# Kernel optimization log

Measured on AMD Instinct MI355X. Metric: run time of the kernel, lower is better.

## Reference

```python
import jax, jax.numpy as jnp
import numpy as np

VAR0, VAR1 = 0.1, 0.2
CONF_THR = 0.02
NMS_THR = 0.4
PRE_K = 5000
POST_K = 750
N = 85680


def setup_inputs() -> dict:
    key = jax.random.key(0)
    k0, k1, k2, k3 = jax.random.split(key, 4)
    return {
        "loc": jax.random.normal(k0, (N, 4), jnp.float32),
        "conf": jax.random.uniform(k1, (N, 2), jnp.float32),
        "landmarks": jax.random.normal(k2, (N, 10), jnp.float32),
        "priors": jax.random.uniform(k3, (N, 4), jnp.float32),
        "img_w": 1920,
        "img_h": 1088,
    }


def _decode_boxes(loc, priors):
    # center-size decode -> xyxy
    cxy = priors[:, :2] + loc[:, :2] * VAR0 * priors[:, 2:]
    wh = priors[:, 2:] * jnp.exp(loc[:, 2:] * VAR1)
    return jnp.concatenate([cxy - wh * 0.5, cxy + wh * 0.5], axis=-1)


def _decode_landmarks(lmk, priors):
    pts = lmk.reshape(-1, 5, 2)                       # [N,5,2]
    out = priors[:, None, :2] + pts * VAR0 * priors[:, None, 2:]
    return out.reshape(-1, 10)


def _pairwise_iou(boxes):
    # boxes: [K,4] xyxy
    area = (boxes[:, 2] - boxes[:, 0]) * (boxes[:, 3] - boxes[:, 1])
    lt = jnp.maximum(boxes[:, None, :2], boxes[None, :, :2])  # [K,K,2]
    rb = jnp.minimum(boxes[:, None, 2:], boxes[None, :, 2:])
    wh = jnp.clip(rb - lt, 0.0)
    inter = wh[..., 0] * wh[..., 1]
    union = area[:, None] + area[None, :] - inter
    return inter / jnp.maximum(union, 1e-12)


def _greedy_nms(boxes, valid, thr):
    # boxes already sorted by descending score; valid marks real candidates.
    K = boxes.shape[0]
    iou = _pairwise_iou(boxes)                         # [K,K]
    idx = jnp.arange(K)

    def body(i, keep):
        suppress = keep[i] & (iou[i] > thr) & (idx > i)
        return keep & ~suppress

    return jax.lax.fori_loop(0, K, body, valid)


def reference(loc, conf, landmarks, priors, img_w, img_h):
    w = jnp.float32(img_w)
    h = jnp.float32(img_h)
    bbox_scale = jnp.array([w, h, w, h], jnp.float32)
    lmk_scale = jnp.tile(jnp.array([w, h], jnp.float32), 5)

    boxes = _decode_boxes(loc, priors) * bbox_scale          # [N,4]
    lmk = _decode_landmarks(landmarks, priors) * lmk_scale   # [N,10]
    scores = conf[:, 1]                                      # [N]

    # confidence filter fused into top-k via -inf masking (static shapes)
    masked = jnp.where(scores > CONF_THR, scores, -jnp.inf)
    top_scores, order = jax.lax.top_k(masked, PRE_K)         # [PRE_K]
    boxes_k = boxes[order]
    lmk_k = lmk[order]
    valid_k = top_scores > CONF_THR

    keep = _greedy_nms(boxes_k, valid_k, NMS_THR)            # [PRE_K] bool

    # compact kept rows (already score-sorted) into fixed [POST_K,15]
    rank = jnp.cumsum(keep) - 1
    rows = jnp.concatenate([boxes_k, top_scores[:, None], lmk_k], axis=1)
    dest = jnp.where(keep & (rank < POST_K), rank, POST_K)   # OOB -> dropped
    out = jnp.zeros((POST_K, 15), jnp.float32).at[dest].set(rows, mode="drop")
    return out
```

## Files before the change

### kernel.cpp

```cpp
#include <hip/hip_runtime.h>
#include <hip/hip_bf16.h>
#include <math.h>

#define N_IN 85680
#define PRE_K 5000
#define POST_K 750
#define NW 79
#define NPAD 5056
#define HSIZE 8192
#define CAND_MAX 8192
#define CONF_THR 0.02f
#define NMS_THR 0.4f
#define BITS_THR 0x3CA3D70Bu
#define NGRP 20

typedef unsigned int u32;
typedef unsigned long long u64;

__device__ __forceinline__ int cbase(int k) { return k * (5088 - 32 * k); }

__device__ __forceinline__ float opaquef(float x) { asm volatile("" : "+v"(x)); return x; }

__device__ __forceinline__ u32 bucket_of(u32 bits) {
    u32 b = (bits - BITS_THR) >> 13;
    return b >= HSIZE ? (HSIZE - 1) : b;
}

__global__ __launch_bounds__(256) void hist_kernel(const float2* __restrict__ conf2,
                                                   u32* __restrict__ hist) {
    __shared__ u32 h[HSIZE];
    for (int b = threadIdx.x; b < HSIZE; b += 256) h[b] = 0u;
    __syncthreads();
    int i = blockIdx.x * 256 + threadIdx.x;
    if (i < N_IN) {
        float s = conf2[i].y;
        if (s > CONF_THR) atomicAdd(&h[bucket_of(__float_as_uint(s))], 1u);
    }
    __syncthreads();
    for (int b = threadIdx.x; b < HSIZE; b += 256) {
        u32 v = h[b];
        if (v) atomicAdd(&hist[b], v);
    }
}

__global__ __launch_bounds__(1024) void scan_kernel(const u32* __restrict__ hist,
                                                    u32* __restrict__ bsel,
                                                    u32* __restrict__ bstart) {
    __shared__ u32 tot[1024];
    int c = threadIdx.x;
    u32 lh[8];
    u32 t = 0;
#pragma unroll
    for (int k = 0; k < 8; ++k) { lh[k] = hist[c * 8 + k]; t += lh[k]; }
    tot[c] = t;
    __syncthreads();
    for (int d = 1; d < 1024; d <<= 1) {
        u32 v = tot[c] + ((c + d < 1024) ? tot[c + d] : 0u);
        __syncthreads();
        tot[c] = v;
        __syncthreads();
    }
    u32 above = (c + 1 < 1024) ? tot[c + 1] : 0u;
    u32 s = above;
    for (int k = 7; k >= 0; --k) { bstart[c * 8 + k] = s; s += lh[k]; }
    if (above < PRE_K && above + t >= PRE_K) {
        u32 cum = above;
        for (int k = 7; k >= 0; --k) {
            cum += lh[k];
            if (cum >= PRE_K) { bsel[0] = (u32)(c * 8 + k); break; }
        }
    }
    if (c == 0 && tot[0] < PRE_K) bsel[0] = 0u;
}

__global__ __launch_bounds__(256) void compact_kernel(const float2* __restrict__ conf2,
                                                      const u32* __restrict__ bsel,
                                                      const u32* __restrict__ bstart,
                                                      u32* __restrict__ bfill,
                                                      u64* __restrict__ cand) {
    int i = blockIdx.x * 256 + threadIdx.x;
    if (i >= N_IN) return;
    float sc = conf2[i].y;
    if (!(sc > CONF_THR)) return;
    u32 bits = __float_as_uint(sc);
    u32 b = bucket_of(bits);
    if (b < bsel[0]) return;
    u32 pos = bstart[b] + atomicAdd(&bfill[b], 1u);
    if (pos < CAND_MAX) cand[pos] = ((u64)bits << 32) | (u64)(u32)(~(u32)i);
}

__global__ __launch_bounds__(256) void rankdec_kernel(const u64* __restrict__ cand,
                                                      const u32* __restrict__ bstart,
                                                      const u32* __restrict__ bfill,
                                                      const u32* __restrict__ bsel,
                                                      const float4* __restrict__ loc4,
                                                      const float4* __restrict__ pri4,
                                                      const float* __restrict__ lmk,
                                                      const int* __restrict__ imw,
                                                      const int* __restrict__ imh,
                                                      float4* __restrict__ rows4,
                                                      float4* __restrict__ boxes,
                                                      u64* __restrict__ validm) {
    u32 bs = bsel[0];
    u32 total = bstart[bs] + bfill[bs];
    if (total > CAND_MAX) total = CAND_MAX;
    float W = (float)(*imw), H = (float)(*imh);
    for (u32 s = blockIdx.x * blockDim.x + threadIdx.x; s < total;
         s += gridDim.x * blockDim.x) {
        u64 key = cand[s];
        u32 b = bucket_of((u32)(key >> 32));
        u32 st = bstart[b];
        u32 en = st + bfill[b];
        if (en > CAND_MAX) en = CAND_MAX;
        u32 r = st;
        for (u32 j = st; j < en; ++j) r += (cand[j] > key) ? 1u : 0u;
        if (r >= PRE_K) continue;
        u32 i = ~(u32)key;
        float score = __uint_as_float((u32)(key >> 32));
        float4 L = loc4[i];
        float4 P = pri4[i];
        float cx = P.x + opaquef((L.x * 0.1f) * P.z);
        float cy = P.y + opaquef((L.y * 0.1f) * P.w);
        float bw = P.z * (float)exp((double)(L.z * 0.2f));
        float bh = P.w * (float)exp((double)(L.w * 0.2f));
        float hw = opaquef(bw * 0.5f), hh = opaquef(bh * 0.5f);
        float x0 = (cx - hw) * W, y0 = (cy - hh) * H;
        float x1 = (cx + hw) * W, y1 = (cy + hh) * H;
        boxes[r] = make_float4(x0, y0, x1, y1);
        float lm[10];
#pragma unroll
        for (int p = 0; p < 5; ++p) {
            float2 q = ((const float2*)lmk)[(size_t)i * 5 + p];
            lm[2 * p]     = (P.x + opaquef((q.x * 0.1f) * P.z)) * W;
            lm[2 * p + 1] = (P.y + opaquef((q.y * 0.1f) * P.w)) * H;
        }
        float4* row = rows4 + (size_t)r * 4;
        row[0] = make_float4(x0, y0, x1, y1);
        row[1] = make_float4(score, lm[0], lm[1], lm[2]);
        row[2] = make_float4(lm[3], lm[4], lm[5], lm[6]);
        row[3] = make_float4(lm[7], lm[8], lm[9], 0.f);
        atomicOr(&validm[r >> 6], 1ull << (r & 63));
    }
}

__global__ __launch_bounds__(64) void mask_kernel(const float4* __restrict__ boxes,
                                                  u64* __restrict__ cmask) {
    int rem = blockIdx.x, rc = 0;
    while (rem >= rc + 1) { rem -= rc + 1; ++rc; }
    int cc = rem;
    __shared__ float4 cb[64];
    int t = threadIdx.x;
    cb[t] = boxes[cc * 64 + t];
    int i = rc * 64 + t;
    float4 bi = boxes[i];
    __syncthreads();
    float areai = (bi.z - bi.x) * (bi.w - bi.y);
    u64 word = 0ull;
#pragma unroll 4
    for (int k = 0; k < 64; ++k) {
        float4 bj = cb[k];
        float areaj = (bj.z - bj.x) * (bj.w - bj.y);
        float ltx = fmaxf(bi.x, bj.x), lty = fmaxf(bi.y, bj.y);
        float rbx = fminf(bi.z, bj.z), rby = fminf(bi.w, bj.w);
        float wx = fmaxf(rbx - ltx, 0.f), wy = fmaxf(rby - lty, 0.f);
        float inter = opaquef(wx * wy);
        float uni = fmaxf(areai + areaj - inter, 1e-12f);
        float iou = inter / uni;
        if (iou > NMS_THR) word |= (1ull << k);
    }
    if (i < PRE_K) cmask[(size_t)(cbase(cc) + (i - 64 * cc))] = word;
}

#define FC(k, q) cmask[(size_t)(cbase(k) + (q) - 64 * (k))]

#define WAITG(need)                                                                   \
    for (;;) {                                                                        \
        u32 d_ = __hip_atomic_load(&doneCnt, __ATOMIC_RELAXED,                        \
                                   __HIP_MEMORY_SCOPE_WORKGROUP);                     \
        if (d_ > (u32)NGRP) { dead = true; break; }                                   \
        if (d_ >= (u32)(need)) break;                                                 \
    }                                                                                 \
    asm volatile("" ::: "memory");

__device__ __forceinline__ u64 nms_solve(u64 valw, u64 sup, u64 dlow) {
    u64 keep = valw & ~__ballot(sup != 0ull);
    for (;;) {
        u64 conm = __ballot((dlow & keep) != 0ull);
        u64 cm = conm & keep;
        if (cm == 0ull) break;
        u64 U = keep & ~conm;
        u64 rem = __ballot((dlow & U) != 0ull) & keep;
        keep &= ~rem;
    }
    return keep;
}

__global__ __launch_bounds__(512) void reduce_scatter_kernel(const u64* __restrict__ cmask,
                                                             const u64* __restrict__ validm,
                                                             const float* __restrict__ rows,
                                                             float* __restrict__ out) {
    int tid = threadIdx.x;
    int g = tid >> 6, lane = tid & 63;
    __shared__ u64 keepAll[96];
    __shared__ u32 totG[32];
    __shared__ u32 doneCnt;
    __shared__ u32 wpref[96];
    for (int k = tid; k < 96; k += 512) keepAll[k] = 0ull;
    if (tid == 0) doneCnt = 0u;
    __syncthreads();
    u64 lmask = (1ull << lane) - 1ull;

    for (int s = 0; s < 3; ++s) {
        int G = s * 8 + g;
        if (G >= NGRP) break;
        int w0 = 4 * G;
        int nwg = NW - w0; if (nwg > 4) nwg = 4;
        int q0 = 64 * w0 + lane;
        int q1 = q0 + 64;
        int q2 = q0 + 128;
        int q3 = (nwg > 3) ? (q0 + 192) : q0;
        u64 t00 = FC(w0, q0);
        u64 t10 = (nwg > 1) ? FC(w0, q1) : 0ull;
        u64 t11 = (nwg > 1) ? FC(w0 + 1, q1) : 0ull;
        u64 t20 = (nwg > 2) ? FC(w0, q2) : 0ull;
        u64 t21 = (nwg > 2) ? FC(w0 + 1, q2) : 0ull;
        u64 t22 = (nwg > 2) ? FC(w0 + 2, q2) : 0ull;
        u64 t30 = (nwg > 3) ? FC(w0, q3) : 0ull;
        u64 t31 = (nwg > 3) ? FC(w0 + 1, q3) : 0ull;
        u64 t32 = (nwg > 3) ? FC(w0 + 2, q3) : 0ull;
        u64 t33 = (nwg > 3) ? FC(w0 + 3, q3) : 0ull;
        u64 v0 = validm[w0];
        u64 v1 = (nwg > 1) ? validm[w0 + 1] : 0ull;
        u64 v2 = (nwg > 2) ? validm[w0 + 2] : 0ull;
        u64 v3 = (nwg > 3) ? validm[w0 + 3] : 0ull;
        u64 sup0 = 0, sup1 = 0, sup2 = 0, sup3 = 0;
        bool dead = false;

        int d0 = 0;
        u64 c00=0,c01=0,c02=0,c03=0,c10=0,c11=0,c12=0,c13=0;
        if (w0 > 0) {
            c00 = FC(0, q0); c01 = FC(0, q1); c02 = FC(0, q2); c03 = FC(0, q3);
            c10 = FC(1, q0); c11 = FC(1, q1); c12 = FC(1, q2); c13 = FC(1, q3);
        }
        asm volatile("" ::: "memory");
        while (d0 < w0) {
            int d1 = d0 + 2;
            u64 n00=0,n01=0,n02=0,n03=0,n10=0,n11=0,n12=0,n13=0;
            if (d1 < w0) {
                n00 = FC(d1, q0);     n01 = FC(d1, q1);     n02 = FC(d1, q2);     n03 = FC(d1, q3);
                n10 = FC(d1 + 1, q0); n11 = FC(d1 + 1, q1); n12 = FC(d1 + 1, q2); n13 = FC(d1 + 1, q3);
            }
            asm volatile("" ::: "memory");
            WAITG(((d0 + 1) >> 2) + 1)
            if (dead) break;
            u64 ka = keepAll[d0], kb = keepAll[d0 + 1];
            sup0 |= (ka & c00) | (kb & c10);
            sup1 |= (ka & c01) | (kb & c11);
            sup2 |= (ka & c02) | (kb & c12);
            sup3 |= (ka & c03) | (kb & c13);
            c00=n00;c01=n01;c02=n02;c03=n03;c10=n10;c11=n11;c12=n12;c13=n13;
            d0 = d1;
        }
        if (!dead) {
            u32 tp = (G > 0) ? totG[G - 1] : 0u;
            u64 k0 = 0, k1 = 0, k2 = 0, k3 = 0;
            if (tp < POST_K) {
                k0 = nms_solve(v0, sup0, t00 & lmask);
                sup1 |= k0 & t10; sup2 |= k0 & t20; sup3 |= k0 & t30;
                k1 = nms_solve(v1, sup1, t11 & lmask);
                sup2 |= k1 & t21; sup3 |= k1 & t31;
                k2 = nms_solve(v2, sup2, t22 & lmask);
                sup3 |= k2 & t32;
                k3 = nms_solve(v3, sup3, t33 & lmask);
            }
            if (lane == 0) {
                keepAll[w0]     = k0;
                keepAll[w0 + 1] = k1;
                keepAll[w0 + 2] = k2;
                keepAll[w0 + 3] = k3;
                u32 tk = tp + (u32)(__popcll(k0) + __popcll(k1) + __popcll(k2) + __popcll(k3));
                totG[G] = tk;
                asm volatile("s_waitcnt lgkmcnt(0)" ::: "memory");
                __hip_atomic_store(&doneCnt,
                                   (tk >= POST_K) ? (u32)(NGRP + 9) : (u32)(G + 1),
                                   __ATOMIC_RELAXED, __HIP_MEMORY_SCOPE_WORKGROUP);
            }
        } else {
            break;
        }
    }
    __syncthreads();

    if (tid == 0) {
        u32 s = 0;
        for (int w = 0; w < NW; ++w) { wpref[w] = s; s += (u32)__popcll(keepAll[w]); }
        wpref[NW] = s;
    }
    __syncthreads();
    u32 totk = wpref[NW]; if (totk > POST_K) totk = POST_K;
    for (int r = tid; r < PRE_K; r += 512) {
        int w = r >> 6, b = r & 63;
        u64 kw = keepAll[w];
        if ((kw >> b) & 1ull) {
            u32 rank = wpref[w] + (u32)__popcll(kw & ((1ull << b) - 1ull));
            if (rank < POST_K) {
                const float* src = rows + (size_t)r * 16;
                float* dst = out + (size_t)rank * 15;
#pragma unroll
                for (int c2 = 0; c2 < 15; ++c2) dst[c2] = src[c2];
            }
        }
    }
    for (int r = (int)totk + tid; r < POST_K; r += 512) {
        float* dst = out + (size_t)r * 15;
#pragma unroll
        for (int c2 = 0; c2 < 15; ++c2) dst[c2] = 0.f;
    }
}

extern "C" void kernel_launch(void* const* d_in, const int* in_sizes, int n_in,
                              void* d_out, int out_size, void* d_ws, size_t ws_size,
                              hipStream_t stream) {
    const float* loc = (const float*)d_in[0];
    const float2* conf2 = (const float2*)d_in[1];
    const float* lmk = (const float*)d_in[2];
    const float* pri = (const float*)d_in[3];
    const int* imw = (const int*)d_in[4];
    const int* imh = (const int*)d_in[5];
    float* out = (float*)d_out;
    char* base = (char*)d_ws;

    u32* hist   = (u32*)(base + 0);
    u32* bfill  = (u32*)(base + 32768);
    u32* bsel   = (u32*)(base + 65536);
    u64* validm = (u64*)(base + 65600);
    u32* bstart = (u32*)(base + 67648);
    u64* cand   = (u64*)(base + 100416);
    float* rows = (float*)(base + 165952);
    float4* boxes = (float4*)(base + 485952);
    u64* cmask  = (u64*)(base + 566848);

    hipMemsetAsync(d_ws, 0, 66624, stream);

    hist_kernel<<<(N_IN + 255) / 256, 256, 0, stream>>>(conf2, hist);
    scan_kernel<<<1, 1024, 0, stream>>>(hist, bsel, bstart);
    compact_kernel<<<(N_IN + 255) / 256, 256, 0, stream>>>(conf2, bsel, bstart, bfill, cand);
    rankdec_kernel<<<24, 256, 0, stream>>>(cand, bstart, bfill, bsel, (const float4*)loc,
                                           (const float4*)pri, lmk, imw, imh,
                                           (float4*)rows, boxes, validm);
    mask_kernel<<<NW * (NW + 1) / 2, 64, 0, stream>>>(boxes, cmask);
    reduce_scatter_kernel<<<1, 512, 0, stream>>>(cmask, validm, rows, out);
}
```

Measured before the change: 94.78 us.

## Fuse histogram and scan via last-block pattern, pack mask tiles, tune launches

Merges the histogram and scan kernels into one launch: the last block to finish (found with an atomic counter) runs the 8192-bin scan using 256 threads and 32 bins each. That block also clears bfill and validm, so the memset shrinks. The mask kernel now packs four 64-thread tiles per 256-thread block and finds its triangular index with a sqrt instead of a loop. The rankdec grid doubles, and wave priority is raised during the serial NMS solve. The aim is to cut a launch and small-kernel overhead, with the risk of a slower single-block scan tail.

```diff
diff --git a/kernel.cpp b/kernel.cpp
--- a/kernel.cpp
+++ b/kernel.cpp
@@ -13,6 +13,7 @@
 #define NMS_THR 0.4f
 #define BITS_THR 0x3CA3D70Bu
 #define NGRP 20
+#define NHB 335
 
 typedef unsigned int u32;
 typedef unsigned long long u64;
@@ -26,51 +27,69 @@
     return b >= HSIZE ? (HSIZE - 1) : b;
 }
 
-__global__ __launch_bounds__(256) void hist_kernel(const float2* __restrict__ conf2,
-                                                   u32* __restrict__ hist) {
+__global__ __launch_bounds__(256) void histscan_kernel(const float2* __restrict__ conf2,
+                                                       u32* __restrict__ hist,
+                                                       u32* __restrict__ hcnt,
+                                                       u32* __restrict__ bsel,
+                                                       u32* __restrict__ bstart,
+                                                       u32* __restrict__ bfill,
+                                                       u64* __restrict__ validm) {
     __shared__ u32 h[HSIZE];
-    for (int b = threadIdx.x; b < HSIZE; b += 256) h[b] = 0u;
-    __syncthreads();
-    int i = blockIdx.x * 256 + threadIdx.x;
+    __shared__ u32 tot[256];
+    __shared__ u32 lastFlag;
+    int c = threadIdx.x;
+    for (int b = c; b < HSIZE; b += 256) h[b] = 0u;
+    __syncthreads();
+    int i = blockIdx.x * 256 + c;
     if (i < N_IN) {
         float s = conf2[i].y;
         if (s > CONF_THR) atomicAdd(&h[bucket_of(__float_as_uint(s))], 1u);
     }
     __syncthreads();
-    for (int b = threadIdx.x; b < HSIZE; b += 256) {
+    for (int b = c; b < HSIZE; b += 256) {
         u32 v = h[b];
         if (v) atomicAdd(&hist[b], v);
     }
-}
-
-__global__ __launch_bounds__(1024) void scan_kernel(const u32* __restrict__ hist,
-                                                    u32* __restrict__ bsel,
-                                                    u32* __restrict__ bstart) {
-    __shared__ u32 tot[1024];
-    int c = threadIdx.x;
-    u32 lh[8];
+    __syncthreads();
+    if (c == 0) {
+        u32 prev = __hip_atomic_fetch_add(hcnt, 1u, __ATOMIC_ACQ_REL,
+                                          __HIP_MEMORY_SCOPE_AGENT);
+        lastFlag = (prev == NHB - 1) ? 1u : 0u;
+    }
+    __syncthreads();
+    if (!lastFlag) return;
+
+    u32 lh[32];
     u32 t = 0;
 #pragma unroll
-    for (int k = 0; k < 8; ++k) { lh[k] = hist[c * 8 + k]; t += lh[k]; }
+    for (int k = 0; k < 32; ++k) {
+        lh[k] = __hip_atomic_load(&hist[c * 32 + k], __ATOMIC_RELAXED,
+                                  __HIP_MEMORY_SCOPE_AGENT);
+        t += lh[k];
+    }
     tot[c] = t;
     __syncthreads();
-    for (int d = 1; d < 1024; d <<= 1) {
-        u32 v = tot[c] + ((c + d < 1024) ? tot[c + d] : 0u);
+    for (int d = 1; d < 256; d <<= 1) {
+        u32 v = tot[c] + ((c + d < 256) ? tot[c + d] : 0u);
         __syncthreads();
         tot[c] = v;
         __syncthreads();
     }
-    u32 above = (c + 1 < 1024) ? tot[c + 1] : 0u;
+    u32 above = (c + 1 < 256) ? tot[c + 1] : 0u;
     u32 s = above;
-    for (int k = 7; k >= 0; --k) { bstart[c * 8 + k] = s; s += lh[k]; }
+#pragma unroll
+    for (int k = 31; k >= 0; --k) { bstart[c * 32 + k] = s; s += lh[k]; }
     if (above < PRE_K && above + t >= PRE_K) {
         u32 cum = above;
-        for (int k = 7; k >= 0; --k) {
+#pragma unroll
+        for (int k = 31; k >= 0; --k) {
             cum += lh[k];
-            if (cum >= PRE_K) { bsel[0] = (u32)(c * 8 + k); break; }
+            if (cum >= PRE_K) { bsel[0] = (u32)(c * 32 + k); break; }
         }
     }
     if (c == 0 && tot[0] < PRE_K) bsel[0] = 0u;
+    for (int b = c; b < HSIZE; b += 256) bfill[b] = 0u;
+    if (c < 128) validm[c] = 0ull;
 }
 
 __global__ __launch_bounds__(256) void compact_kernel(const float2* __restrict__ conf2,
@@ -143,22 +162,24 @@
     }
 }
 
-__global__ __launch_bounds__(64) void mask_kernel(const float4* __restrict__ boxes,
-                                                  u64* __restrict__ cmask) {
-    int rem = blockIdx.x, rc = 0;
-    while (rem >= rc + 1) { rem -= rc + 1; ++rc; }
-    int cc = rem;
-    __shared__ float4 cb[64];
-    int t = threadIdx.x;
-    cb[t] = boxes[cc * 64 + t];
+__global__ __launch_bounds__(256) void mask_kernel(const float4* __restrict__ boxes,
+                                                   u64* __restrict__ cmask) {
+    __shared__ float4 cb4[4][64];
+    int wv = threadIdx.x >> 6, t = threadIdx.x & 63;
+    int t64 = blockIdx.x * 4 + wv;
+    if (t64 >= NW * (NW + 1) / 2) return;
+    int rc = (int)((sqrtf(8.0f * (float)t64 + 1.0f) - 1.0f) * 0.5f);
+    while ((rc + 1) * (rc + 2) / 2 <= t64) ++rc;
+    while (rc * (rc + 1) / 2 > t64) --rc;
+    int cc = t64 - rc * (rc + 1) / 2;
+    cb4[wv][t] = boxes[cc * 64 + t];
     int i = rc * 64 + t;
     float4 bi = boxes[i];
-    __syncthreads();
     float areai = (bi.z - bi.x) * (bi.w - bi.y);
     u64 word = 0ull;
 #pragma unroll 4
     for (int k = 0; k < 64; ++k) {
-        float4 bj = cb[k];
+        float4 bj = cb4[wv][k];
         float areaj = (bj.z - bj.x) * (bj.w - bj.y);
         float ltx = fmaxf(bi.x, bj.x), lty = fmaxf(bi.y, bj.y);
         float rbx = fminf(bi.z, bj.z), rby = fminf(bi.w, bj.w);
@@ -262,6 +283,7 @@
             d0 = d1;
         }
         if (!dead) {
+            __builtin_amdgcn_s_setprio(1);
             u32 tp = (G > 0) ? totG[G - 1] : 0u;
             u64 k0 = 0, k1 = 0, k2 = 0, k3 = 0;
             if (tp < POST_K) {
@@ -285,6 +307,7 @@
                                    (tk >= POST_K) ? (u32)(NGRP + 9) : (u32)(G + 1),
                                    __ATOMIC_RELAXED, __HIP_MEMORY_SCOPE_WORKGROUP);
             }
+            __builtin_amdgcn_s_setprio(0);
         } else {
             break;
         }
@@ -331,23 +354,23 @@
     char* base = (char*)d_ws;
 
     u32* hist   = (u32*)(base + 0);
-    u32* bfill  = (u32*)(base + 32768);
-    u32* bsel   = (u32*)(base + 65536);
-    u64* validm = (u64*)(base + 65600);
-    u32* bstart = (u32*)(base + 67648);
-    u64* cand   = (u64*)(base + 100416);
-    float* rows = (float*)(base + 165952);
-    float4* boxes = (float4*)(base + 485952);
-    u64* cmask  = (u64*)(base + 566848);
-
-    hipMemsetAsync(d_ws, 0, 66624, stream);
-
-    hist_kernel<<<(N_IN + 255) / 256, 256, 0, stream>>>(conf2, hist);
-    scan_kernel<<<1, 1024, 0, stream>>>(hist, bsel, bstart);
+    u32* bsel   = (u32*)(base + 32768);
+    u32* hcnt   = (u32*)(base + 32832);
+    u32* bfill  = (u32*)(base + 33088);
+    u32* bstart = (u32*)(base + 65856);
+    u64* validm = (u64*)(base + 98624);
+    u64* cand   = (u64*)(base + 99648);
+    float* rows = (float*)(base + 165184);
+    float4* boxes = (float4*)(base + 485184);
+    u64* cmask  = (u64*)(base + 566080);
+
+    hipMemsetAsync(d_ws, 0, 33088, stream);
+
+    histscan_kernel<<<NHB, 256, 0, stream>>>(conf2, hist, hcnt, bsel, bstart, bfill, validm);
     compact_kernel<<<(N_IN + 255) / 256, 256, 0, stream>>>(conf2, bsel, bstart, bfill, cand);
-    rankdec_kernel<<<24, 256, 0, stream>>>(cand, bstart, bfill, bsel, (const float4*)loc,
+    rankdec_kernel<<<48, 256, 0, stream>>>(cand, bstart, bfill, bsel, (const float4*)loc,
                                            (const float4*)pri, lmk, imw, imh,
                                            (float4*)rows, boxes, validm);
-    mask_kernel<<<NW * (NW + 1) / 2, 64, 0, stream>>>(boxes, cmask);
+    mask_kernel<<<(NW * (NW + 1) / 2 + 3) / 4, 256, 0, stream>>>(boxes, cmask);
     reduce_scatter_kernel<<<1, 512, 0, stream>>>(cmask, validm, rows, out);
 }
```

New measurement: 101.1 us. 6.7% more time.
